# Performance work log

Measured on AMD Instinct MI355X. Metric: run time of the kernel, lower is better.

Reference implementation:

```python
import jax, jax.numpy as jnp
import numpy as np

EPS = 1e-7
NUM_HEADS = 16

def _ln(x, g, b):
    m = jnp.mean(x, -1, keepdims=True)
    v = jnp.var(x, -1, keepdims=True)
    return (x - m) * jax.lax.rsqrt(v + EPS) * g + b

def _gelu(x):
    return jax.nn.gelu(x, approximate=False)  # torch nn.GELU default = exact erf

def _attn(x, qkv_w, qkv_b, pw, pb):
    B, N, C = x.shape
    D = C // NUM_HEADS
    qkv = (x @ qkv_w.T + qkv_b).reshape(B, N, 3, NUM_HEADS, D).transpose(2, 0, 3, 1, 4)
    q, k, v = qkv[0], qkv[1], qkv[2]
    a = jax.nn.softmax(jnp.einsum('bhnd,bhmd->bhnm', q, k) * (D ** -0.5), axis=-1)
    o = jnp.einsum('bhnm,bhmd->bhnd', a, v).transpose(0, 2, 1, 3).reshape(B, N, C)
    return o @ pw.T + pb

def _gcn(x, w, b, adj):
    # x: (B,C,J); w: (C*K,C) 1x1 conv, then einsum 'nkctv,kvw->nctw' with t==1
    K = adj.shape[0]
    B, C, J = x.shape
    y = jnp.einsum('bcj,oc->boj', x, w) + b[None, :, None]
    y = y.reshape(B, K, C, J)
    return jnp.einsum('bkcv,kvw->bcw', y, adj)

def _mlp(x, w1, b1, w2, b2):
    return _gelu(_gelu(x @ w1.T + b1) @ w2.T + b2)

def _lrsc(x, adj, l1g, l1b, l2g, l2b, g1w, g1b, g2w, g2b, m1w, m1b, m2w, m2b):
    x = x.transpose(0, 2, 1)                       # (B,C,J)
    res = x
    xn = _ln(x, l1g, l1b)                          # LayerNorm over J
    x = res + _mlp(xn, m1w, m1b, m2w, m2b) + _gcn(xn, g1w, g1b, adj)
    x = _ln(x.transpose(0, 2, 1), l2g, l2b).transpose(0, 2, 1)  # LayerNorm over C
    res = x
    x = res + _mlp(x, m1w, m1b, m2w, m2b) + _gcn(x, g2w, g2b, adj)
    return x.transpose(0, 2, 1)                    # (B,J,C)

def _gkpc(x, lg, lb, q1w, q1b, p1w, p1b, q2w, q2b, p2w, p2b):
    x = x + _attn(_ln(x, lg, lb), q1w, q1b, p1w, p1b)
    return _attn(_ln(x, lg, lb), q2w, q2b, p2w, p2b)  # note: no residual on second attn

def _forward(x, adj, ln1_g, ln1_b, ln2_g, ln2_b, gcn1_w, gcn1_b, gcn2_w, gcn2_b,
             mlp1_w1, mlp1_b1, mlp1_w2, mlp1_b2, attn_ln_g, attn_ln_b,
             qkv1_w, qkv1_b, proj1_w, proj1_b, qkv2_w, qkv2_b, proj2_w, proj2_b,
             tn_g, tn_b):
    L = ln1_g.shape[0]
    for i in range(L):
        # GG_ACM/RR_ACM/LCM are published as identity -> both 0.3/0.7 mixes equal x + gelu(x)
        xin = x + _gelu(x)
        x5 = _gkpc(xin, attn_ln_g[i], attn_ln_b[i], qkv1_w[i], qkv1_b[i],
                   proj1_w[i], proj1_b[i], qkv2_w[i], qkv2_b[i], proj2_w[i], proj2_b[i])
        x7 = _lrsc(xin, adj, ln1_g[i], ln1_b[i], ln2_g[i], ln2_b[i],
                   gcn1_w[i], gcn1_b[i], gcn2_w[i], gcn2_b[i],
                   mlp1_w1[i], mlp1_b1[i], mlp1_w2[i], mlp1_b2[i])
        x = x + x5 + x7
    return _ln(x, tn_g, tn_b)

def setup_inputs():
    B, V, C, K, L = 2048, 17, 512, 3, 3
    s = 0.05
    ks = jax.random.split(jax.random.key(0), 12)
    rn = lambda k, sh: jax.random.normal(k, sh, jnp.float32) * s
    return dict(
        x=jax.random.normal(ks[0], (B, V, C), jnp.float32),
        adj=jax.random.uniform(ks[1], (K, V, V), dtype=jnp.float32),
        ln1_g=jnp.ones((L, V), jnp.float32), ln1_b=jnp.zeros((L, V), jnp.float32),
        ln2_g=jnp.ones((L, C), jnp.float32), ln2_b=jnp.zeros((L, C), jnp.float32),
        gcn1_w=rn(ks[2], (L, C * K, C)), gcn1_b=jnp.zeros((L, C * K), jnp.float32),
        gcn2_w=rn(ks[3], (L, C * K, C)), gcn2_b=jnp.zeros((L, C * K), jnp.float32),
        mlp1_w1=rn(ks[4], (L, C, V)), mlp1_b1=jnp.zeros((L, C), jnp.float32),
        mlp1_w2=rn(ks[5], (L, V, C)), mlp1_b2=jnp.zeros((L, V), jnp.float32),
        attn_ln_g=jnp.ones((L, C), jnp.float32), attn_ln_b=jnp.zeros((L, C), jnp.float32),
        qkv1_w=rn(ks[6], (L, 3 * C, C)), qkv1_b=jnp.zeros((L, 3 * C), jnp.float32),
        proj1_w=rn(ks[7], (L, C, C)), proj1_b=jnp.zeros((L, C), jnp.float32),
        qkv2_w=rn(ks[8], (L, 3 * C, C)), qkv2_b=jnp.zeros((L, 3 * C), jnp.float32),
        proj2_w=rn(ks[9], (L, C, C)), proj2_b=jnp.zeros((L, C), jnp.float32),
        tn_g=jnp.ones((C,), jnp.float32), tn_b=jnp.zeros((C,), jnp.float32),
    )

def reference(x, adj, ln1_g, ln1_b, ln2_g, ln2_b, gcn1_w, gcn1_b, gcn2_w, gcn2_b,
              mlp1_w1, mlp1_b1, mlp1_w2, mlp1_b2, attn_ln_g, attn_ln_b,
              qkv1_w, qkv1_b, proj1_w, proj1_b, qkv2_w, qkv2_b, proj2_w, proj2_b,
              tn_g, tn_b):
    return _forward(x, adj, ln1_g, ln1_b, ln2_g, ln2_b, gcn1_w, gcn1_b, gcn2_w, gcn2_b,
                    mlp1_w1, mlp1_b1, mlp1_w2, mlp1_b2, attn_ln_g, attn_ln_b,
                    qkv1_w, qkv1_b, proj1_w, proj1_b, qkv2_w, qkv2_b, proj2_w, proj2_b,
                    tn_g, tn_b)
```

## Files before the change

### kernel.cpp

```cpp
#include <hip/hip_runtime.h>
#include <hip/hip_bf16.h>
#include <math.h>

#define Bn 2048
#define Vn 17
#define Cn 512
static const size_t NE = (size_t)Bn * Vn * Cn;
#define MROWS (Bn * Vn)

typedef __attribute__((ext_vector_type(8))) short bf16x8;
typedef __attribute__((ext_vector_type(4))) short bf16x4;
typedef __attribute__((ext_vector_type(4))) float f32x4;
typedef __attribute__((ext_vector_type(2))) unsigned int u32x2;
typedef unsigned short u16;

__device__ __forceinline__ float u2f(u16 u) { return __uint_as_float(((unsigned)u) << 16); }
__device__ __forceinline__ u16 f2u(float f) {
    unsigned u = __float_as_uint(f);
    return (u16)((u + 0x7fffu + ((u >> 16) & 1u)) >> 16);
}
__device__ __forceinline__ float gelu_f(float x) {
    return 0.5f * x * (1.0f + erff(x * 0.70710678118654752f));
}
__device__ __forceinline__ float exp2_raw(float x) {
    float r; asm("v_exp_f32 %0, %1" : "=v"(r) : "v"(x)); return r;
}
__device__ __forceinline__ float gelu_fast(float x) {
    float b = x * fmaf(x * x, -0.10294348f, -2.30220820f);
    return x * __builtin_amdgcn_rcpf(1.0f + exp2_raw(b));
}
__device__ __forceinline__ unsigned cvtpk(float lo, float hi) {
    unsigned r; asm("v_cvt_pk_bf16_f32 %0, %1, %2" : "=v"(r) : "v"(lo), "v"(hi)); return r;
}
__device__ __forceinline__ bf16x4 gelupk(f32x4 v) {
    u32x2 t = {cvtpk(gelu_fast(v[0]), gelu_fast(v[1])), cvtpk(gelu_fast(v[2]), gelu_fast(v[3]))};
    return __builtin_bit_cast(bf16x4, t);
}
__device__ __forceinline__ f32x4 mfma16(bf16x4 a, bf16x4 b, f32x4 c) {
    asm("v_mfma_f32_16x16x16_bf16 %0, %1, %2, %0" : "+v"(c) : "v"(a), "v"(b));
    return c;
}
__device__ __forceinline__ void gload16(const u16* g, u16* l) {
    __builtin_amdgcn_global_load_lds((const __attribute__((address_space(1))) void*)g,
                                     (__attribute__((address_space(3))) void*)l, 16, 0, 0);
}

__global__ void k_diag(float* __restrict__ o, float v, int n) {
    int i = blockIdx.x * 256 + threadIdx.x;
    if (i < n) o[i] = v;
}

__global__ void k_f2b(const float4* __restrict__ s, ushort4* __restrict__ d, int n4) {
    int i = blockIdx.x * 256 + threadIdx.x;
    if (i >= n4) return;
    float4 v = s[i];
    ushort4 o = {f2u(v.x), f2u(v.y), f2u(v.z), f2u(v.w)};
    d[i] = o;
}

__global__ void k_mpad(const float* __restrict__ W1, const float* __restrict__ W2,
                       u16* __restrict__ W1p, u16* __restrict__ W2p) {
    int t = blockIdx.x * 256 + threadIdx.x;
    if (t < 512 * 32) {
        int o = t >> 5, j = t & 31;
        W1p[t] = (j < 17) ? f2u(W1[o * 17 + j]) : (u16)0;
    } else {
        int t2 = t - 512 * 32;
        int w = t2 >> 9;
        W2p[t2] = (w < 17) ? f2u(W2[t2]) : (u16)0;
    }
}

__global__ void k_xingelu(const float* __restrict__ X, u16* __restrict__ O, int n8) {
    int i = blockIdx.x * 256 + threadIdx.x;
    if (i >= n8) return;
    float4 a = *(const float4*)(X + (size_t)i * 8);
    float4 b = *(const float4*)(X + (size_t)i * 8 + 4);
    float v[8] = {a.x, a.y, a.z, a.w, b.x, b.y, b.z, b.w};
    bf16x8 r;
#pragma unroll
    for (int k = 0; k < 8; k++) r[k] = f2u(v[k] + gelu_f(v[k]));
    *(bf16x8*)(O + (size_t)i * 8) = r;
}

template <int F32IO>
__global__ __launch_bounds__(256) void k_ln_c(const void* __restrict__ Xv,
                                              const float* __restrict__ g,
                                              const float* __restrict__ bt,
                                              void* __restrict__ Ov, int nrows) {
    int row = blockIdx.x * 4 + (threadIdx.x >> 6);
    if (row >= nrows) return;
    int lane = threadIdx.x & 63;
    float vv[8];
    if (F32IO) {
        const float* xp = (const float*)Xv + (size_t)row * Cn + lane * 8;
        float4 v0 = *(const float4*)xp, v1 = *(const float4*)(xp + 4);
        vv[0] = v0.x; vv[1] = v0.y; vv[2] = v0.z; vv[3] = v0.w;
        vv[4] = v1.x; vv[5] = v1.y; vv[6] = v1.z; vv[7] = v1.w;
    } else {
        bf16x8 h = *(const bf16x8*)((const u16*)Xv + (size_t)row * Cn + lane * 8);
#pragma unroll
        for (int k = 0; k < 8; k++) vv[k] = u2f((u16)h[k]);
    }
    float s = 0.f, q = 0.f;
#pragma unroll
    for (int k = 0; k < 8; k++) { s += vv[k]; q = fmaf(vv[k], vv[k], q); }
#pragma unroll
    for (int o = 32; o; o >>= 1) { s += __shfl_xor(s, o); q += __shfl_xor(q, o); }
    float mean = s * (1.f / Cn);
    float var = q * (1.f / Cn) - mean * mean;
    float inv = 1.f / sqrtf(var + 1e-7f);
    int cb = lane * 8;
    if (F32IO) {
        float r[8];
#pragma unroll
        for (int k = 0; k < 8; k++) r[k] = (vv[k] - mean) * inv * g[cb + k] + bt[cb + k];
        float* op = (float*)Ov + (size_t)row * Cn + cb;
        *(float4*)op = make_float4(r[0], r[1], r[2], r[3]);
        *(float4*)(op + 4) = make_float4(r[4], r[5], r[6], r[7]);
    } else {
        bf16x8 r;
#pragma unroll
        for (int k = 0; k < 8; k++) r[k] = f2u((vv[k] - mean) * inv * g[cb + k] + bt[cb + k]);
        *(bf16x8*)((u16*)Ov + (size_t)row * Cn + cb) = r;
    }
}

__global__ __launch_bounds__(256) void k_ln_j(const u16* __restrict__ X,
                                              const float* __restrict__ g,
                                              const float* __restrict__ bt,
                                              u16* __restrict__ O) {
    int idx = blockIdx.x * 256 + threadIdx.x;
    int b = idx >> 9, c = idx & 511;
    const u16* xp = X + (size_t)b * Vn * Cn + c;
    float v[Vn];
    float s = 0.f;
#pragma unroll
    for (int j = 0; j < Vn; j++) { v[j] = u2f(xp[(size_t)j * Cn]); s += v[j]; }
    float mean = s * (1.f / Vn);
    float q = 0.f;
#pragma unroll
    for (int j = 0; j < Vn; j++) { float d = v[j] - mean; q = fmaf(d, d, q); }
    float inv = 1.f / sqrtf(q * (1.f / Vn) + 1e-7f);
    u16* op = O + (size_t)b * Vn * Cn + c;
#pragma unroll
    for (int j = 0; j < Vn; j++) op[(size_t)j * Cn] = f2u((v[j] - mean) * inv * g[j] + bt[j]);
}

template <int REMAP, int EPI>
__global__ __launch_bounds__(256) void k_gemm(const u16* __restrict__ A, const u16* __restrict__ W,
                                              const float* __restrict__ bias, u16* __restrict__ OutB,
                                              const u16* __restrict__ Res, float* __restrict__ Xf,
                                              int hbase, int shift) {
    constexpr int NT = REMAP ? 6 : 8;
    const int K = 512;
    int wave = threadIdx.x >> 6, lane = threadIdx.x & 63;
    int m0 = blockIdx.x * 128 + wave * 32;
    int nbase = blockIdx.y * (16 * NT);
    int r16 = lane & 15, kq = lane >> 4;
    int ld = REMAP ? (3 << shift) : 512;

    const u16* wp[NT];
    int wrow[NT];
#pragma unroll
    for (int nt = 0; nt < NT; nt++) {
        int n = nbase + nt * 16 + r16;
        int wr;
        if (REMAP) {
            int s = n >> shift, off = n & ((1 << shift) - 1);
            wr = (s << 9) + hbase + off;
        } else wr = n;
        wrow[nt] = wr;
        wp[nt] = W + (size_t)wr * K + kq * 8;
    }
    f32x4 acc[2][NT];
#pragma unroll
    for (int i = 0; i < 2; i++)
#pragma unroll
        for (int nt = 0; nt < NT; nt++) acc[i][nt] = (f32x4){0.f, 0.f, 0.f, 0.f};

    const u16* ap = A + (size_t)(m0 + r16) * K + kq * 8;
    for (int k0 = 0; k0 < K; k0 += 32) {
        bf16x8 a0 = *(const bf16x8*)(ap + k0);
        bf16x8 a1 = *(const bf16x8*)(ap + (size_t)16 * K + k0);
#pragma unroll
        for (int nt = 0; nt < NT; nt++) {
            bf16x8 bf = *(const bf16x8*)(wp[nt] + k0);
            acc[0][nt] = __builtin_amdgcn_mfma_f32_16x16x32_bf16(a0, bf, acc[0][nt], 0, 0, 0);
            acc[1][nt] = __builtin_amdgcn_mfma_f32_16x16x32_bf16(a1, bf, acc[1][nt], 0, 0, 0);
        }
    }
#pragma unroll
    for (int nt = 0; nt < NT; nt++) {
        float bv = bias[wrow[nt]];
        int n = nbase + nt * 16 + r16;
#pragma unroll
        for (int i = 0; i < 2; i++) {
#pragma unroll
            for (int r = 0; r < 4; r++) {
                size_t mb = (size_t)(m0 + i * 16 + kq * 4 + r);
                float v = acc[i][nt][r] + bv;
                if (EPI == 0) OutB[mb * ld + n] = f2u(v);
                else if (EPI == 1) { size_t o = mb * 512 + n; OutB[o] = f2u(v + u2f(Res[o])); }
                else { size_t o = mb * 512 + n; Xf[o] += v; }
            }
        }
    }
}

template <int EPI, int NY>
__global__ __launch_bounds__(256) void k_gemm2(const u16* __restrict__ A, const u16* __restrict__ W,
                                               const float* __restrict__ bias, u16* __restrict__ OutB,
                                               const u16* __restrict__ Res, float* __restrict__ Xf,
                                               int N) {
    __shared__ u16 As[128 * 64];
    __shared__ u16 Bs[128 * 64];
    const int K = 512;
    int tid = threadIdx.x;
    int wave = tid >> 6, lane = tid & 63;
    int cpx = gridDim.x >> 3;
    int bid = blockIdx.x;
    int swz = (bid & 7) * cpx + (bid >> 3);
    int m0 = (swz / NY) * 128, n0 = (swz % NY) * 128;
    int r16 = lane & 15, kq = lane >> 4;

    int srow = wave << 2;
    int lrow = lane >> 3;
    int lcol = (lane & 7) * 8;

    f32x4 acc[2][8];
#pragma unroll
    for (int i = 0; i < 2; i++)
#pragma unroll
        for (int j = 0; j < 8; j++) acc[i][j] = (f32x4){0.f, 0.f, 0.f, 0.f};

    const u16* aT = As + (wave * 32 + r16) * 64 + kq * 8;
    const u16* bT = Bs + r16 * 64 + kq * 8;

    for (int k0 = 0; k0 < K; k0 += 64) {
#pragma unroll
        for (int i = 0; i < 4; i++) {
            int rows = (srow + i) * 8 + lrow;
            gload16(A + (size_t)(m0 + rows) * K + k0 + lcol, (u16*)As + (srow + i) * 512);
            gload16(W + (size_t)(n0 + rows) * K + k0 + lcol, (u16*)Bs + (srow + i) * 512);
        }
        __syncthreads();
#pragma unroll
        for (int kk = 0; kk < 64; kk += 32) {
            bf16x8 af0 = *(const bf16x8*)(aT + kk);
            bf16x8 af1 = *(const bf16x8*)(aT + 16 * 64 + kk);
#pragma unroll
            for (int nt = 0; nt < 8; nt++) {
                bf16x8 bf = *(const bf16x8*)(bT + nt * 16 * 64 + kk);
                acc[0][nt] = __builtin_amdgcn_mfma_f32_16x16x32_bf16(af0, bf, acc[0][nt], 0, 0, 0);
                acc[1][nt] = __builtin_amdgcn_mfma_f32_16x16x32_bf16(af1, bf, acc[1][nt], 0, 0, 0);
            }
        }
        __syncthreads();
    }

    int mw = m0 + wave * 32;
#pragma unroll
    for (int nt = 0; nt < 8; nt++) {
        int n = n0 + nt * 16 + r16;
        float bv = bias[n];
#pragma unroll
        for (int i = 0; i < 2; i++) {
#pragma unroll
            for (int r = 0; r < 4; r++) {
                size_t mb = (size_t)(mw + i * 16 + kq * 4 + r);
                size_t o = mb * N + n;
                float v = acc[i][nt][r] + bv;
                if (EPI == 0) OutB[o] = f2u(v);
                else if (EPI == 1) OutB[o] = f2u(v + u2f(Res[o]));
                else Xf[o] += v;
            }
        }
    }
}

__global__ __launch_bounds__(256) void k_attn(const u16* __restrict__ Y, u16* __restrict__ T,
                                              int shift, int hgbase, int l2ch) {
    int wv = threadIdx.x >> 6, lane = threadIdx.x & 63;
    if (lane >= 34) return;
    int gw = blockIdx.x * 4 + wv;
    int which = (lane >= 17) ? 1 : 0;
    int j = lane - which * 17;
    int pid = gw * 2 + which;
    int b = pid >> l2ch;
    int hl = pid & ((1 << l2ch) - 1);
    int CW = 1 << shift;
    int row3 = 3 << shift;

    const u16* qb = Y + (size_t)(b * Vn + j) * row3 + hl * 32;
    float q[32];
#pragma unroll
    for (int d0 = 0; d0 < 32; d0 += 8) {
        bf16x8 h = *(const bf16x8*)(qb + d0);
#pragma unroll
        for (int d = 0; d < 8; d++) q[d0 + d] = u2f((u16)h[d]);
    }
    float sc[Vn];
    float mx = -1e30f;
#pragma unroll
    for (int kk = 0; kk < Vn; kk++) {
        const u16* kb = Y + (size_t)(b * Vn + kk) * row3 + CW + hl * 32;
        float s = 0.f;
#pragma unroll
        for (int d0 = 0; d0 < 32; d0 += 8) {
            bf16x8 h = *(const bf16x8*)(kb + d0);
#pragma unroll
            for (int d = 0; d < 8; d++) s = fmaf(q[d0 + d], u2f((u16)h[d]), s);
        }
        s *= 0.1767766952966369f;
        sc[kk] = s;
        mx = fmaxf(mx, s);
    }
    float sum = 0.f;
#pragma unroll
    for (int kk = 0; kk < Vn; kk++) { sc[kk] = __expf(sc[kk] - mx); sum += sc[kk]; }
    float inv = 1.f / sum;
    float o[32];
#pragma unroll
    for (int d = 0; d < 32; d++) o[d] = 0.f;
#pragma unroll
    for (int kk = 0; kk < Vn; kk++) {
        const u16* vb = Y + (size_t)(b * Vn + kk) * row3 + 2 * CW + hl * 32;
        float p = sc[kk] * inv;
#pragma unroll
        for (int d0 = 0; d0 < 32; d0 += 8) {
            bf16x8 h = *(const bf16x8*)(vb + d0);
#pragma unroll
            for (int d = 0; d < 8; d++) o[d0 + d] = fmaf(p, u2f((u16)h[d]), o[d0 + d]);
        }
    }
    u16* op = T + (size_t)(b * Vn + j) * Cn + hgbase + hl * 32;
#pragma unroll
    for (int d0 = 0; d0 < 32; d0 += 8) {
        bf16x8 r;
#pragma unroll
        for (int d = 0; d < 8; d++) r[d] = f2u(o[d0 + d]);
        *(bf16x8*)(op + d0) = r;
    }
}

template <int MODE>
__global__ __launch_bounds__(256) void k_agg(const u16* __restrict__ Y, const float* __restrict__ Adj,
                                             const u16* __restrict__ aux1, const u16* __restrict__ aux2,
                                             u16* __restrict__ OutB, float* __restrict__ Xf,
                                             int cbase, int shift) {
    __shared__ float adj_s[3][Vn][Vn];
    for (int t = threadIdx.x; t < 3 * Vn * Vn; t += 256) {
        int k = t / (Vn * Vn), r = t - k * Vn * Vn;
        adj_s[k][r / Vn][r % Vn] = Adj[t];
    }
    __syncthreads();
    int CW = 1 << shift;
    int idx = blockIdx.x * 256 + threadIdx.x;
    int b = idx >> shift, co = idx & (CW - 1);
    int c = cbase + co;
    int row3 = 3 << shift;
    float acc[Vn];
#pragma unroll
    for (int w = 0; w < Vn; w++) acc[w] = 0.f;
    const u16* yb = Y + (size_t)b * Vn * row3 + co;
#pragma unroll
    for (int k = 0; k < 3; k++)
#pragma unroll
        for (int v = 0; v < Vn; v++) {
            float y = u2f(yb[(size_t)v * row3 + k * CW]);
#pragma unroll
            for (int w = 0; w < Vn; w++) acc[w] = fmaf(y, adj_s[k][v][w], acc[w]);
        }
    size_t rb = (size_t)(b * Vn) * Cn + c;
#pragma unroll
    for (int w = 0; w < Vn; w++) {
        size_t o = rb + (size_t)w * Cn;
        float val = acc[w] + u2f(aux1[o]) + u2f(aux2[o]);
        if (MODE == 0) OutB[o] = f2u(val);
        else Xf[o] += val;
    }
}

__global__ __launch_bounds__(512) void k_mlp(const u16* __restrict__ X,
                                             const u16* __restrict__ W1p, const float* __restrict__ B1,
                                             const u16* __restrict__ W2p, const float* __restrict__ B2,
                                             u16* __restrict__ O) {
    __shared__ u16 Xs[256 * 40];
    __shared__ float B1s[512];
    int b = blockIdx.x >> 1;
    int cbase = (blockIdx.x & 1) << 8;
    int tid = threadIdx.x;

    for (int i = tid; i < 256 * 40 / 8; i += 512) ((float4*)Xs)[i] = make_float4(0.f, 0.f, 0.f, 0.f);
    if (tid < 128) ((float4*)B1s)[tid] = ((const float4*)B1)[tid];
    __syncthreads();
    const u16* xb = X + (size_t)b * (Vn * Cn) + cbase;
    for (int i = tid; i < 17 * 256; i += 512) {
        int j = i >> 8, c = i & 255;
        Xs[c * 40 + j] = xb[j * Cn + c];
    }
    __syncthreads();

    int wave = tid >> 6, lane = tid & 63;
    int r16 = lane & 15, kq = lane >> 4;
    int crow = wave * 32;

    bf16x8 xf0 = *(const bf16x8*)(Xs + (crow + r16) * 40 + kq * 8);
    bf16x8 xf1 = *(const bf16x8*)(Xs + (crow + 16 + r16) * 40 + kq * 8);

    f32x4 acc2[2][2];
#pragma unroll
    for (int i = 0; i < 2; i++)
#pragma unroll
        for (int j = 0; j < 2; j++) acc2[i][j] = (f32x4){0.f, 0.f, 0.f, 0.f};

    for (int s = 0; s < 16; s++) {
        const u16* w1p = W1p + ((s * 32 + r16) << 5) + kq * 8;
        bf16x8 af0 = *(const bf16x8*)w1p;
        bf16x8 af1 = *(const bf16x8*)(w1p + 16 * 32);
        f32x4 bi0 = *(const f32x4*)(B1s + s * 32 + kq * 4);
        f32x4 bi1 = *(const f32x4*)(B1s + s * 32 + 16 + kq * 4);
        f32x4 a00 = __builtin_amdgcn_mfma_f32_16x16x32_bf16(af0, xf0, bi0, 0, 0, 0);
        f32x4 a01 = __builtin_amdgcn_mfma_f32_16x16x32_bf16(af0, xf1, bi0, 0, 0, 0);
        f32x4 a10 = __builtin_amdgcn_mfma_f32_16x16x32_bf16(af1, xf0, bi1, 0, 0, 0);
        f32x4 a11 = __builtin_amdgcn_mfma_f32_16x16x32_bf16(af1, xf1, bi1, 0, 0, 0);
        bf16x4 p00 = gelupk(a00);
        bf16x4 p01 = gelupk(a01);
        bf16x4 p10 = gelupk(a10);
        bf16x4 p11 = gelupk(a11);
        const u16* w2p = W2p + (size_t)r16 * 512 + s * 32 + kq * 4;
        bf16x4 wb00 = *(const bf16x4*)(w2p);
        bf16x4 wb01 = *(const bf16x4*)(w2p + 16);
        bf16x4 wb10 = *(const bf16x4*)(w2p + 16 * 512);
        bf16x4 wb11 = *(const bf16x4*)(w2p + 16 * 512 + 16);
        acc2[0][0] = mfma16(p00, wb00, acc2[0][0]);
        acc2[0][0] = mfma16(p10, wb01, acc2[0][0]);
        acc2[1][0] = mfma16(p01, wb00, acc2[1][0]);
        acc2[1][0] = mfma16(p11, wb01, acc2[1][0]);
        acc2[0][1] = mfma16(p00, wb10, acc2[0][1]);
        acc2[0][1] = mfma16(p10, wb11, acc2[0][1]);
        acc2[1][1] = mfma16(p01, wb10, acc2[1][1]);
        acc2[1][1] = mfma16(p11, wb11, acc2[1][1]);
    }

    u16* ob = O + (size_t)b * (Vn * Cn) + cbase;
    float bb0 = B2[r16];
#pragma unroll
    for (int cg = 0; cg < 2; cg++) {
        int cl = crow + cg * 16 + kq * 4;
        f32x4 v = acc2[cg][0];
        uint2 pk = make_uint2(cvtpk(gelu_fast(v[0] + bb0), gelu_fast(v[1] + bb0)),
                              cvtpk(gelu_fast(v[2] + bb0), gelu_fast(v[3] + bb0)));
        *(uint2*)(ob + (size_t)r16 * Cn + cl) = pk;
        if (r16 == 0) {
            float bb1 = B2[16];
            f32x4 w = acc2[cg][1];
            uint2 pk1 = make_uint2(cvtpk(gelu_fast(w[0] + bb1), gelu_fast(w[1] + bb1)),
                                   cvtpk(gelu_fast(w[2] + bb1), gelu_fast(w[3] + bb1)));
            *(uint2*)(ob + (size_t)16 * Cn + cl) = pk1;
        }
    }
}

extern "C" void kernel_launch(void* const* d_in, const int* in_sizes, int n_in,
                              void* d_out, int out_size, void* d_ws, size_t ws_size,
                              hipStream_t stream) {
    (void)in_sizes; (void)n_in; (void)out_size;
    typedef const float* fp;
    fp x_in = (fp)d_in[0];
    fp adj = (fp)d_in[1];
    fp ln1_g = (fp)d_in[2], ln1_b = (fp)d_in[3];
    fp ln2_g = (fp)d_in[4], ln2_b = (fp)d_in[5];
    fp gcn1_w = (fp)d_in[6], gcn1_b = (fp)d_in[7];
    fp gcn2_w = (fp)d_in[8], gcn2_b = (fp)d_in[9];
    fp m1w = (fp)d_in[10], m1b = (fp)d_in[11];
    fp m2w = (fp)d_in[12], m2b = (fp)d_in[13];
    fp aln_g = (fp)d_in[14], aln_b = (fp)d_in[15];
    fp qkv1_w = (fp)d_in[16], qkv1_b = (fp)d_in[17];
    fp p1w = (fp)d_in[18], p1b = (fp)d_in[19];
    fp qkv2_w = (fp)d_in[20], qkv2_b = (fp)d_in[21];
    fp p2w = (fp)d_in[22], p2b = (fp)d_in[23];
    fp tn_g = (fp)d_in[24], tn_b = (fp)d_in[25];

    const size_t NE2 = NE * 2;
    const size_t WSCR_SZ = (size_t)1536 * 512 * 2;
    const size_t MPAD_SZ = (size_t)(512 * 32 + 32 * 512) * 2;

    int CH = 0;
    for (int ch = 16; ch >= 1; ch >>= 1) {
        size_t need = 3 * NE2 + WSCR_SZ + MPAD_SZ + (size_t)MROWS * 96 * ch * 2 + 1024;
        if (need <= ws_size) { CH = ch; break; }
    }
    if (!CH) {
        k_diag<<<(int)((NE + 255) / 256), 256, 0, stream>>>((float*)d_out, (float)ws_size, (int)NE);
        return;
    }
    const int l2ch = __builtin_ctz(CH);
    const int shift = 5 + l2ch;
    const int NCH = 16 / CH;
    const bool FAST = (CH == 16);

    char* p = (char*)d_ws;
    u16* XIN = (u16*)p;  p += NE2;
    u16* T1 = (u16*)p;   p += NE2;
    u16* T2 = (u16*)p;   p += NE2;
    u16* YCH = (u16*)p;  p += (size_t)MROWS * 96 * CH * 2;
    u16* WSCR = (u16*)p; p += WSCR_SZ;
    u16* MPAD1 = (u16*)p;
    u16* MPAD2 = MPAD1 + 512 * 32;

    float* X = (float*)d_out;
    hipMemcpyAsync(X, x_in, NE * 4, hipMemcpyDeviceToDevice, stream);

    const int G8 = (int)(NE / 8 / 256);
    const int GLN = MROWS / 4;
    const int GBC = Bn * Cn / 256;
    const int GATT = (Bn << l2ch) / 8;
    const int GAGG = (Bn << shift) / 256;
    const dim3 GEMM_C(MROWS / 128, CH);
    const dim3 GEMM_P(MROWS / 128, 4);
    const int CV_QKV = (int)(1536 * 512 / 4 / 256);
    const int CV_P = (int)(512 * 512 / 4 / 256);
    const int GQF = (MROWS / 128) * 12;
    const int GPF = (MROWS / 128) * 4;

    for (int i = 0; i < 3; i++) {
        fp q1w = qkv1_w + (size_t)i * 1536 * 512, q1b = qkv1_b + i * 1536;
        fp q2w = qkv2_w + (size_t)i * 1536 * 512, q2b = qkv2_b + i * 1536;
        fp g1w = gcn1_w + (size_t)i * 1536 * 512, g1b = gcn1_b + i * 1536;
        fp g2w = gcn2_w + (size_t)i * 1536 * 512, g2b = gcn2_b + i * 1536;
        fp pw1 = p1w + (size_t)i * 512 * 512, pb1 = p1b + i * Cn;
        fp pw2 = p2w + (size_t)i * 512 * 512, pb2 = p2b + i * Cn;
        fp alg = aln_g + i * Cn, alb = aln_b + i * Cn;
        fp l1g = ln1_g + i * Vn, l1b_ = ln1_b + i * Vn;
        fp l2g = ln2_g + i * Cn, l2b_ = ln2_b + i * Cn;
        fp w1 = m1w + (size_t)i * Cn * Vn, b1 = m1b + i * Cn;
        fp w2 = m2w + (size_t)i * Vn * Cn, b2 = m2b + i * Vn;

        k_xingelu<<<G8, 256, 0, stream>>>(X, XIN, (int)(NE / 8));
        k_mpad<<<128, 256, 0, stream>>>(w1, w2, MPAD1, MPAD2);

        k_ln_c<0><<<GLN, 256, 0, stream>>>(XIN, alg, alb, T1, MROWS);
        k_f2b<<<CV_QKV, 256, 0, stream>>>((const float4*)q1w, (ushort4*)WSCR, 1536 * 512 / 4);
        if (FAST) {
            k_gemm2<0, 12><<<GQF, 256, 0, stream>>>(T1, WSCR, q1b, YCH, nullptr, nullptr, 1536);
            k_attn<<<GATT, 256, 0, stream>>>(YCH, T2, shift, 0, l2ch);
        } else {
            for (int hg = 0; hg < NCH; hg++) {
                k_gemm<1, 0><<<GEMM_C, 256, 0, stream>>>(T1, WSCR, q1b, YCH, nullptr, nullptr, hg << shift, shift);
                k_attn<<<GATT, 256, 0, stream>>>(YCH, T2, shift, hg << shift, l2ch);
            }
        }
        k_f2b<<<CV_P, 256, 0, stream>>>((const float4*)pw1, (ushort4*)WSCR, 512 * 512 / 4);
        if (FAST) k_gemm2<1, 4><<<GPF, 256, 0, stream>>>(T2, WSCR, pb1, T1, XIN, nullptr, 512);
        else k_gemm<0, 1><<<GEMM_P, 256, 0, stream>>>(T2, WSCR, pb1, T1, XIN, nullptr, 0, 0);
        k_ln_c<0><<<GLN, 256, 0, stream>>>(T1, alg, alb, T2, MROWS);
        k_f2b<<<CV_QKV, 256, 0, stream>>>((const float4*)q2w, (ushort4*)WSCR, 1536 * 512 / 4);
        if (FAST) {
            k_gemm2<0, 12><<<GQF, 256, 0, stream>>>(T2, WSCR, q2b, YCH, nullptr, nullptr, 1536);
            k_attn<<<GATT, 256, 0, stream>>>(YCH, T1, shift, 0, l2ch);
        } else {
            for (int hg = 0; hg < NCH; hg++) {
                k_gemm<1, 0><<<GEMM_C, 256, 0, stream>>>(T2, WSCR, q2b, YCH, nullptr, nullptr, hg << shift, shift);
                k_attn<<<GATT, 256, 0, stream>>>(YCH, T1, shift, hg << shift, l2ch);
            }
        }
        k_f2b<<<CV_P, 256, 0, stream>>>((const float4*)pw2, (ushort4*)WSCR, 512 * 512 / 4);
        if (FAST) k_gemm2<2, 4><<<GPF, 256, 0, stream>>>(T1, WSCR, pb2, nullptr, nullptr, X, 512);
        else k_gemm<0, 2><<<GEMM_P, 256, 0, stream>>>(T1, WSCR, pb2, nullptr, nullptr, X, 0, 0);

        k_ln_j<<<GBC, 256, 0, stream>>>(XIN, l1g, l1b_, T1);
        k_mlp<<<Bn * 2, 512, 0, stream>>>(T1, MPAD1, b1, MPAD2, b2, T2);
        k_f2b<<<CV_QKV, 256, 0, stream>>>((const float4*)g1w, (ushort4*)WSCR, 1536 * 512 / 4);
        if (FAST) {
            k_gemm2<0, 12><<<GQF, 256, 0, stream>>>(T1, WSCR, g1b, YCH, nullptr, nullptr, 1536);
            k_agg<0><<<GAGG, 256, 0, stream>>>(YCH, adj, XIN, T2, XIN, nullptr, 0, shift);
        } else {
            for (int cc = 0; cc < NCH; cc++) {
                k_gemm<1, 0><<<GEMM_C, 256, 0, stream>>>(T1, WSCR, g1b, YCH, nullptr, nullptr, cc << shift, shift);
                k_agg<0><<<GAGG, 256, 0, stream>>>(YCH, adj, XIN, T2, XIN, nullptr, cc << shift, shift);
            }
        }
        k_ln_c<0><<<GLN, 256, 0, stream>>>(XIN, l2g, l2b_, T1, MROWS);
        k_mlp<<<Bn * 2, 512, 0, stream>>>(T1, MPAD1, b1, MPAD2, b2, T2);
        k_f2b<<<CV_QKV, 256, 0, stream>>>((const float4*)g2w, (ushort4*)WSCR, 1536 * 512 / 4);
        if (FAST) {
            k_gemm2<0, 12><<<GQF, 256, 0, stream>>>(T1, WSCR, g2b, YCH, nullptr, nullptr, 1536);
            k_agg<1><<<GAGG, 256, 0, stream>>>(YCH, adj, T1, T2, nullptr, X, 0, shift);
        } else {
            for (int cc = 0; cc < NCH; cc++) {
                k_gemm<1, 0><<<GEMM_C, 256, 0, stream>>>(T1, WSCR, g2b, YCH, nullptr, nullptr, cc << shift, shift);
                k_agg<1><<<GAGG, 256, 0, stream>>>(YCH, adj, T1, T2, nullptr, X, cc << shift, shift);
            }
        }
    }

    k_ln_c<1><<<GLN, 256, 0, stream>>>(X, tn_g, tn_b, X, MROWS);
}
```

Measured before the change: 4.397 ms.

## Prefetch MLP weights one step ahead and use MFMA/exp builtins instead of asm

The fused MLP kernel loop now loads the next step's W1, W2 and bias fragments before issuing the current step's MFMAs (register double-buffering), fully unrolls the loop and interleaves the second-stage MFMAs to break dependency chains. Inline asm for v_exp, v_cvt_pk_bf16 and the 16x16x16 MFMA is replaced with compiler builtins or software rounding, so the compiler can schedule around them and insert hazard waits itself. The cost is more live registers, and the software bf16 rounding adds ALU work compared with the packed convert instruction.

```diff
diff --git a/kernel.cpp b/kernel.cpp
--- a/kernel.cpp
+++ b/kernel.cpp
@@ -11,7 +11,6 @@
 typedef __attribute__((ext_vector_type(8))) short bf16x8;
 typedef __attribute__((ext_vector_type(4))) short bf16x4;
 typedef __attribute__((ext_vector_type(4))) float f32x4;
-typedef __attribute__((ext_vector_type(2))) unsigned int u32x2;
 typedef unsigned short u16;
 
 __device__ __forceinline__ float u2f(u16 u) { return __uint_as_float(((unsigned)u) << 16); }
@@ -22,24 +21,40 @@
 __device__ __forceinline__ float gelu_f(float x) {
     return 0.5f * x * (1.0f + erff(x * 0.70710678118654752f));
 }
-__device__ __forceinline__ float exp2_raw(float x) {
-    float r; asm("v_exp_f32 %0, %1" : "=v"(r) : "v"(x)); return r;
+__device__ __forceinline__ float exp2f_fast(float b) {
+#if __has_builtin(__builtin_amdgcn_exp2f)
+    return __builtin_amdgcn_exp2f(b);
+#else
+    return __expf(b * 0.69314718056f);
+#endif
 }
 __device__ __forceinline__ float gelu_fast(float x) {
     float b = x * fmaf(x * x, -0.10294348f, -2.30220820f);
-    return x * __builtin_amdgcn_rcpf(1.0f + exp2_raw(b));
-}
-__device__ __forceinline__ unsigned cvtpk(float lo, float hi) {
-    unsigned r; asm("v_cvt_pk_bf16_f32 %0, %1, %2" : "=v"(r) : "v"(lo), "v"(hi)); return r;
+    return x * __builtin_amdgcn_rcpf(1.0f + exp2f_fast(b));
 }
 __device__ __forceinline__ bf16x4 gelupk(f32x4 v) {
-    u32x2 t = {cvtpk(gelu_fast(v[0]), gelu_fast(v[1])), cvtpk(gelu_fast(v[2]), gelu_fast(v[3]))};
-    return __builtin_bit_cast(bf16x4, t);
-}
+    bf16x4 r;
+    r[0] = (short)f2u(gelu_fast(v[0]));
+    r[1] = (short)f2u(gelu_fast(v[1]));
+    r[2] = (short)f2u(gelu_fast(v[2]));
+    r[3] = (short)f2u(gelu_fast(v[3]));
+    return r;
+}
+#if __has_builtin(__builtin_amdgcn_mfma_f32_16x16x16bf16_1k)
 __device__ __forceinline__ f32x4 mfma16(bf16x4 a, bf16x4 b, f32x4 c) {
-    asm("v_mfma_f32_16x16x16_bf16 %0, %1, %2, %0" : "+v"(c) : "v"(a), "v"(b));
+    return __builtin_amdgcn_mfma_f32_16x16x16bf16_1k(a, b, c, 0, 0, 0);
+}
+#elif __has_builtin(__builtin_amdgcn_mfma_f32_16x16x16_bf16)
+__device__ __forceinline__ f32x4 mfma16(bf16x4 a, bf16x4 b, f32x4 c) {
+    return __builtin_amdgcn_mfma_f32_16x16x16_bf16(a, b, c, 0, 0, 0);
+}
+#else
+__device__ __forceinline__ f32x4 mfma16(bf16x4 a, bf16x4 b, f32x4 c) {
+    asm volatile("s_nop 2\n\tv_mfma_f32_16x16x16_bf16 %0, %1, %2, %0\n\ts_nop 4"
+                 : "+v"(c) : "v"(a), "v"(b));
     return c;
 }
+#endif
 __device__ __forceinline__ void gload16(const u16* g, u16* l) {
     __builtin_amdgcn_global_load_lds((const __attribute__((address_space(1))) void*)g,
                                      (__attribute__((address_space(3))) void*)l, 16, 0, 0);
@@ -415,12 +430,36 @@
 #pragma unroll
         for (int j = 0; j < 2; j++) acc2[i][j] = (f32x4){0.f, 0.f, 0.f, 0.f};
 
+    const u16* w1b = W1p + (r16 << 5) + kq * 8;
+    const u16* w2b = W2p + (size_t)r16 * 512 + kq * 4;
+    const float* b1b = B1s + kq * 4;
+
+    bf16x8 af0 = *(const bf16x8*)(w1b);
+    bf16x8 af1 = *(const bf16x8*)(w1b + 512);
+    bf16x4 wb00 = *(const bf16x4*)(w2b);
+    bf16x4 wb01 = *(const bf16x4*)(w2b + 16);
+    bf16x4 wb10 = *(const bf16x4*)(w2b + 8192);
+    bf16x4 wb11 = *(const bf16x4*)(w2b + 8192 + 16);
+    f32x4 bi0 = *(const f32x4*)(b1b);
+    f32x4 bi1 = *(const f32x4*)(b1b + 16);
+
+#pragma unroll
     for (int s = 0; s < 16; s++) {
-        const u16* w1p = W1p + ((s * 32 + r16) << 5) + kq * 8;
-        bf16x8 af0 = *(const bf16x8*)w1p;
-        bf16x8 af1 = *(const bf16x8*)(w1p + 16 * 32);
-        f32x4 bi0 = *(const f32x4*)(B1s + s * 32 + kq * 4);
-        f32x4 bi1 = *(const f32x4*)(B1s + s * 32 + 16 + kq * 4);
+        bf16x8 naf0 = af0, naf1 = af1;
+        bf16x4 nwb00 = wb00, nwb01 = wb01, nwb10 = wb10, nwb11 = wb11;
+        f32x4 nbi0 = bi0, nbi1 = bi1;
+        if (s < 15) {
+            const u16* w1n = w1b + (s + 1) * 1024;
+            naf0 = *(const bf16x8*)(w1n);
+            naf1 = *(const bf16x8*)(w1n + 512);
+            const u16* w2n = w2b + (s + 1) * 32;
+            nwb00 = *(const bf16x4*)(w2n);
+            nwb01 = *(const bf16x4*)(w2n + 16);
+            nwb10 = *(const bf16x4*)(w2n + 8192);
+            nwb11 = *(const bf16x4*)(w2n + 8192 + 16);
+            nbi0 = *(const f32x4*)(b1b + (s + 1) * 32);
+            nbi1 = *(const f32x4*)(b1b + (s + 1) * 32 + 16);
+        }
         f32x4 a00 = __builtin_amdgcn_mfma_f32_16x16x32_bf16(af0, xf0, bi0, 0, 0, 0);
         f32x4 a01 = __builtin_amdgcn_mfma_f32_16x16x32_bf16(af0, xf1, bi0, 0, 0, 0);
         f32x4 a10 = __builtin_amdgcn_mfma_f32_16x16x32_bf16(af1, xf0, bi1, 0, 0, 0);
@@ -429,19 +468,17 @@
         bf16x4 p01 = gelupk(a01);
         bf16x4 p10 = gelupk(a10);
         bf16x4 p11 = gelupk(a11);
-        const u16* w2p = W2p + (size_t)r16 * 512 + s * 32 + kq * 4;
-        bf16x4 wb00 = *(const bf16x4*)(w2p);
-        bf16x4 wb01 = *(const bf16x4*)(w2p + 16);
-        bf16x4 wb10 = *(const bf16x4*)(w2p + 16 * 512);
-        bf16x4 wb11 = *(const bf16x4*)(w2p + 16 * 512 + 16);
         acc2[0][0] = mfma16(p00, wb00, acc2[0][0]);
+        acc2[1][0] = mfma16(p01, wb00, acc2[1][0]);
+        acc2[0][1] = mfma16(p00, wb10, acc2[0][1]);
+        acc2[1][1] = mfma16(p01, wb10, acc2[1][1]);
         acc2[0][0] = mfma16(p10, wb01, acc2[0][0]);
-        acc2[1][0] = mfma16(p01, wb00, acc2[1][0]);
         acc2[1][0] = mfma16(p11, wb01, acc2[1][0]);
-        acc2[0][1] = mfma16(p00, wb10, acc2[0][1]);
         acc2[0][1] = mfma16(p10, wb11, acc2[0][1]);
-        acc2[1][1] = mfma16(p01, wb10, acc2[1][1]);
         acc2[1][1] = mfma16(p11, wb11, acc2[1][1]);
+        af0 = naf0; af1 = naf1;
+        wb00 = nwb00; wb01 = nwb01; wb10 = nwb10; wb11 = nwb11;
+        bi0 = nbi0; bi1 = nbi1;
     }
 
     u16* ob = O + (size_t)b * (Vn * Cn) + cbase;
@@ -450,14 +487,16 @@
     for (int cg = 0; cg < 2; cg++) {
         int cl = crow + cg * 16 + kq * 4;
         f32x4 v = acc2[cg][0];
-        uint2 pk = make_uint2(cvtpk(gelu_fast(v[0] + bb0), gelu_fast(v[1] + bb0)),
-                              cvtpk(gelu_fast(v[2] + bb0), gelu_fast(v[3] + bb0)));
+        uint2 pk;
+        pk.x = (unsigned)f2u(gelu_fast(v[0] + bb0)) | ((unsigned)f2u(gelu_fast(v[1] + bb0)) << 16);
+        pk.y = (unsigned)f2u(gelu_fast(v[2] + bb0)) | ((unsigned)f2u(gelu_fast(v[3] + bb0)) << 16);
         *(uint2*)(ob + (size_t)r16 * Cn + cl) = pk;
         if (r16 == 0) {
             float bb1 = B2[16];
             f32x4 w = acc2[cg][1];
-            uint2 pk1 = make_uint2(cvtpk(gelu_fast(w[0] + bb1), gelu_fast(w[1] + bb1)),
-                                   cvtpk(gelu_fast(w[2] + bb1), gelu_fast(w[3] + bb1)));
+            uint2 pk1;
+            pk1.x = (unsigned)f2u(gelu_fast(w[0] + bb1)) | ((unsigned)f2u(gelu_fast(w[1] + bb1)) << 16);
+            pk1.y = (unsigned)f2u(gelu_fast(w[2] + bb1)) | ((unsigned)f2u(gelu_fast(w[3] + bb1)) << 16);
             *(uint2*)(ob + (size_t)16 * Cn + cl) = pk1;
         }
     }
```

Measured after the change: 4.449 ms. No clear change (+1.2%).
